# Performance work log

Hardware: AMD Instinct MI355X
Metric: run time of the kernel (lower is better)

The kernel has to match this reference:

```python
import jax, jax.numpy as jnp
import numpy as np

B, S, HID = 1, 2048, 2048
NH, NKV, HD = 32, 8, 64
SCALE = HD ** -0.5


def _rotary_tables(seq_len, dim, base=10000.0):
    inv_freq = 1.0 / (base ** (jnp.arange(0, dim, 2, dtype=jnp.float32) / dim))
    t = jnp.arange(seq_len, dtype=jnp.float32)
    freqs = jnp.outer(t, inv_freq)                      # [S, D/2]
    emb = jnp.concatenate([freqs, freqs], axis=-1)      # [S, D]
    return jnp.cos(emb)[None], jnp.sin(emb)[None]       # [1, S, D]


def setup_inputs() -> dict:
    key = jax.random.key(0)
    ks = jax.random.split(key, 5)
    cos, sin = _rotary_tables(S, HD)
    std = HID ** -0.5
    return {
        "hidden_states": jax.random.normal(ks[0], (B, S, HID), jnp.float32),
        "cos": cos,
        "sin": sin,
        "Wq": jax.random.normal(ks[1], (HID, NH * HD), jnp.float32) * std,
        "Wk": jax.random.normal(ks[2], (HID, NKV * HD), jnp.float32) * std,
        "Wv": jax.random.normal(ks[3], (HID, NKV * HD), jnp.float32) * std,
        "Wo": jax.random.normal(ks[4], (NH * HD, HID), jnp.float32) * std,
    }


def _rotate_half(x):
    x1, x2 = jnp.split(x, 2, axis=-1)
    return jnp.concatenate([-x2, x1], axis=-1)


def reference(hidden_states, cos, sin, Wq, Wk, Wv, Wo):
    b, s, _ = hidden_states.shape
    # projections -> [B, H, S, D]
    q = (hidden_states @ Wq).reshape(b, s, NH, HD).transpose(0, 2, 1, 3)
    k = (hidden_states @ Wk).reshape(b, s, NKV, HD).transpose(0, 2, 1, 3)
    v = (hidden_states @ Wv).reshape(b, s, NKV, HD).transpose(0, 2, 1, 3)
    # rotary embedding (broadcast over heads)
    c = cos[:, None, :, :]
    sn = sin[:, None, :, :]
    q = q * c + _rotate_half(q) * sn
    k = k * c + _rotate_half(k) * sn
    # GQA: repeat kv heads
    groups = NH // NKV
    k = jnp.repeat(k, groups, axis=1)
    v = jnp.repeat(v, groups, axis=1)
    scores = jnp.einsum("bhqd,bhkd->bhqk", q, k) * SCALE
    causal = jnp.tril(jnp.ones((s, s), dtype=bool))
    scores = jnp.where(causal, scores, jnp.finfo(scores.dtype).min)
    weights = jax.nn.softmax(scores, axis=-1)
    attn = jnp.einsum("bhqk,bhkd->bhqd", weights, v)
    attn = attn.transpose(0, 2, 1, 3).reshape(b, s, NH * HD)
    out = attn @ Wo
    return out, weights
```

## Files before the change

kernel.cpp:

```cpp
#include <hip/hip_runtime.h>

typedef short short8 __attribute__((ext_vector_type(8)));
typedef float f32x4 __attribute__((ext_vector_type(4)));

#define S_LEN 2048
#define HID 2048
#define NH 32
#define NKV 8
#define HD 64
#define DQKV 3072
#define SCALE 0.125f
#define SM_OFF 8.0f

static __device__ __forceinline__ unsigned short f2bf(float f) {
    unsigned int u = __float_as_uint(f);
    u += 0x7FFF + ((u >> 16) & 1);
    return (unsigned short)(u >> 16);
}
static __device__ __forceinline__ float bf2f(unsigned short u) {
    return __uint_as_float((unsigned int)u << 16);
}

#define GLDS16(g, l)                                                                     \
    __builtin_amdgcn_global_load_lds((const __attribute__((address_space(1))) unsigned int*)(g), \
                                     (__attribute__((address_space(3))) unsigned int*)(l), 16, 0, 0)

__global__ void prep(const float* __restrict__ Wq, const float* __restrict__ Wk,
                     const float* __restrict__ Wv, const float* __restrict__ Wo,
                     const float* __restrict__ hidden,
                     unsigned short* __restrict__ Wt, unsigned short* __restrict__ Wot,
                     unsigned short* __restrict__ Hb) {
    const int z = blockIdx.z;
    const int t = threadIdx.x;
    if (z == 4) {
        int idx = (blockIdx.y * 64 + blockIdx.x) * 256 + t;
        float4 v = ((const float4*)hidden)[idx];
        ushort4 o = {f2bf(v.x), f2bf(v.y), f2bf(v.z), f2bf(v.w)};
        ((ushort4*)Hb)[idx] = o;
        return;
    }
    const float* src; unsigned short* dst; int sld;
    if (z == 0)      { src = Wq; dst = Wt; sld = HID; }
    else if (z == 1) { if (blockIdx.x >= 16) return; src = Wk; dst = Wt + (size_t)2048 * HID; sld = 512; }
    else if (z == 2) { if (blockIdx.x >= 16) return; src = Wv; dst = Wt + (size_t)2560 * HID; sld = 512; }
    else             { src = Wo; dst = Wot; sld = HID; }
    __shared__ float tile[32][33];
    const int tx = t & 31, ty = t >> 5;
    const int r0 = blockIdx.y * 32, c0 = blockIdx.x * 32;
#pragma unroll
    for (int i = 0; i < 4; ++i)
        tile[ty * 4 + i][tx] = src[(size_t)(r0 + ty * 4 + i) * sld + c0 + tx];
    __syncthreads();
#pragma unroll
    for (int i = 0; i < 4; ++i)
        dst[(size_t)(c0 + ty * 4 + i) * HID + r0 + tx] = f2bf(tile[tx][ty * 4 + i]);
}

template <int MODE>
__global__ __launch_bounds__(512) void gemm_fused(const unsigned short* __restrict__ A,
                                                  const unsigned short* __restrict__ Bt,
                                                  float* __restrict__ C,
                                                  const float* __restrict__ cosb,
                                                  const float* __restrict__ sinb,
                                                  unsigned short* __restrict__ Qb,
                                                  unsigned short* __restrict__ Kb,
                                                  unsigned short* __restrict__ Vt,
                                                  int K, int lda, int ldb, int ldc) {
    __shared__ __align__(16) unsigned short As[128 * 64];
    __shared__ __align__(16) unsigned short Bs[128 * 64];
    const int t = threadIdx.x, lane = t & 63, wv = t >> 6;
    const int m0 = blockIdx.y * 128, n0 = blockIdx.x * 128;
    const int wm = wv >> 1, wn = wv & 1;
    const int lr = lane & 15, lg = lane >> 4;
    const int srow = lane >> 3;
    const int scol = ((lane & 7) ^ srow) * 8;
    f32x4 acc[2][4] = {};
    for (int k0 = 0; k0 < K; k0 += 64) {
        __syncthreads();
#pragma unroll
        for (int p = 0; p < 2; ++p) {
            int rbase = wv * 16 + p * 8;
            GLDS16(&A[(size_t)(m0 + rbase + srow) * lda + k0 + scol], &As[rbase * 64]);
            GLDS16(&Bt[(size_t)(n0 + rbase + srow) * ldb + k0 + scol], &Bs[rbase * 64]);
        }
        __syncthreads();
#pragma unroll
        for (int kk = 0; kk < 2; ++kk) {
            short8 a[2], b[4];
#pragma unroll
            for (int i = 0; i < 2; ++i) {
                int row = wm * 32 + i * 16 + lr;
                a[i] = *(const short8*)&As[row * 64 + (((kk * 4 + lg) ^ (row & 7)) * 8)];
            }
#pragma unroll
            for (int j = 0; j < 4; ++j) {
                int row = wn * 64 + j * 16 + lr;
                b[j] = *(const short8*)&Bs[row * 64 + (((kk * 4 + lg) ^ (row & 7)) * 8)];
            }
#pragma unroll
            for (int i = 0; i < 2; ++i)
#pragma unroll
                for (int j = 0; j < 4; ++j)
                    acc[i][j] = __builtin_amdgcn_mfma_f32_16x16x32_bf16(a[i], b[j], acc[i][j], 0, 0, 0);
        }
    }

    if (MODE == 1) {
#pragma unroll
        for (int i = 0; i < 2; ++i)
#pragma unroll
            for (int j = 0; j < 4; ++j)
#pragma unroll
                for (int r = 0; r < 4; ++r)
                    C[(size_t)(m0 + wm * 32 + i * 16 + lg * 4 + r) * ldc +
                      n0 + wn * 64 + j * 16 + lr] = acc[i][j][r];
        return;
    }

    const int head = (n0 + wn * 64) >> 6;
    if (head < NH + NKV) {
        unsigned short* dst = (head < NH) ? Qb : Kb;
        const int dld = (head < NH) ? HID : 512;
        const int hc = (head < NH) ? head * HD : (head - NH) * HD;
#pragma unroll
        for (int i = 0; i < 2; ++i) {
            const int s0 = m0 + wm * 32 + i * 16 + lg * 4;
#pragma unroll
            for (int j = 0; j < 2; ++j) {
                const int c = j * 16 + lr;
#pragma unroll
                for (int r = 0; r < 4; ++r) {
                    const int s = s0 + r;
                    float x1 = acc[i][j][r], x2 = acc[i][j + 2][r];
                    float c1 = cosb[s * HD + c],      s1 = sinb[s * HD + c];
                    float c2 = cosb[s * HD + c + 32], s2 = sinb[s * HD + c + 32];
                    dst[(size_t)s * dld + hc + c]      = f2bf(x1 * c1 - x2 * s1);
                    dst[(size_t)s * dld + hc + c + 32] = f2bf(x2 * c2 + x1 * s2);
                }
            }
        }
    } else {
        const int vh = head - NH - NKV;
#pragma unroll
        for (int i = 0; i < 2; ++i) {
            const int s0 = m0 + wm * 32 + i * 16 + lg * 4;
#pragma unroll
            for (int j = 0; j < 4; ++j) {
                const int d = vh * HD + j * 16 + lr;
                ushort4 o = {f2bf(acc[i][j][0]), f2bf(acc[i][j][1]),
                             f2bf(acc[i][j][2]), f2bf(acc[i][j][3])};
                *(ushort4*)&Vt[(size_t)d * S_LEN + s0] = o;
            }
        }
    }
}

#define KSZ (128 * 72)
#define VSZ (64 * 136)
__global__ __launch_bounds__(512) void attn_fused(const unsigned short* __restrict__ Qb,
                                                  const unsigned short* __restrict__ Kb,
                                                  const unsigned short* __restrict__ Vt,
                                                  float* __restrict__ w,
                                                  unsigned short* __restrict__ Ab) {
    __shared__ __align__(16) unsigned short Ks[2 * KSZ];
    __shared__ __align__(16) unsigned short Vs[2 * VSZ];
    __shared__ __align__(16) unsigned short Ps[8][32 * 40];
    const int p = blockIdx.x, h = blockIdx.y, kvh = h >> 2;
    const int t = threadIdx.x, lane = t & 63, wv = t >> 6;
    const int grp = wv & 1, wr = wv >> 1;
    const int qt = grp ? (15 - p) : p;
    const int q0 = qt * 128;
    const int lr = lane & 15, lg = lane >> 4;
    const int ktmax = 15 - p;
    unsigned short* Pw = &Ps[wv][0];

    const float C1 = SCALE;
    const float NEG = -1.0e30f;

    short8 qf[2][2];
#pragma unroll
    for (int i = 0; i < 2; ++i)
#pragma unroll
        for (int kk = 0; kk < 2; ++kk)
            qf[i][kk] = *(const short8*)&Qb[(size_t)(q0 + wr * 32 + i * 16 + lr) * HID +
                                            h * HD + kk * 32 + lg * 8];

    const int krow = t >> 2, kc = (t & 3) * 16;
    const int vrow = t >> 3, vc = (t & 7) * 16;

    short8 kA, kB, vA, vB;
#define LOADK(kt) { const unsigned short* kp = &Kb[(size_t)((kt) * 128 + krow) * 512 + kvh * HD]; \
                    kA = *(const short8*)&kp[kc]; kB = *(const short8*)&kp[kc + 8]; }
#define WRITEK(b) { *(short8*)&Ks[(b) * KSZ + krow * 72 + kc] = kA;                 \
                    *(short8*)&Ks[(b) * KSZ + krow * 72 + kc + 8] = kB; }
#define LOADV(kt) { const unsigned short* vp = &Vt[(size_t)(kvh * HD + vrow) * S_LEN + (kt) * 128]; \
                    vA = *(const short8*)&vp[vc]; vB = *(const short8*)&vp[vc + 8]; }
#define WRITEV(b) { *(short8*)&Vs[(b) * VSZ + vrow * 136 + vc] = vA;                \
                    *(short8*)&Vs[(b) * VSZ + vrow * 136 + vc + 8] = vB; }

    float l_r[2] = {0.f, 0.f};

    LOADK(0); WRITEK(0);
    __syncthreads();
    LOADK(1);
    for (int kt = 0; kt <= ktmax; ++kt) {
        const int b = kt & 1;
        if (kt <= qt) {
            f32x4 acc[8][2] = {};
#pragma unroll
            for (int kk = 0; kk < 2; ++kk) {
                short8 af[8];
#pragma unroll
                for (int j = 0; j < 8; ++j)
                    af[j] = *(const short8*)&Ks[b * KSZ + (j * 16 + lr) * 72 + kk * 32 + lg * 8];
#pragma unroll
                for (int j = 0; j < 8; ++j)
#pragma unroll
                    for (int i = 0; i < 2; ++i)
                        acc[j][i] = __builtin_amdgcn_mfma_f32_16x16x32_bf16(af[j], qf[i][kk], acc[j][i], 0, 0, 0);
            }
            const bool diag = (kt == qt);
#pragma unroll
            for (int i = 0; i < 2; ++i) {
                const int qg = q0 + wr * 32 + i * 16 + lr;
                float sum = 0.f;
#pragma unroll
                for (int j = 0; j < 8; ++j)
#pragma unroll
                    for (int r = 0; r < 4; ++r) {
                        int kg = kt * 128 + j * 16 + lg * 4 + r;
                        float s2 = fmaf(acc[j][i][r], C1, -SM_OFF);
                        s2 = (!diag || kg <= qg) ? s2 : NEG;
                        sum += __expf(s2);
                    }
                sum += __shfl_xor(sum, 16);
                sum += __shfl_xor(sum, 32);
                l_r[i] += sum;
            }
        }
        if (kt < ktmax) WRITEK(b ^ 1);
        __syncthreads();
        if (kt + 2 <= ktmax) LOADK(kt + 2);
    }

    const float invl[2] = {1.f / l_r[0], 1.f / l_r[1]};

    f32x4 o[2][4] = {};
    LOADK(0); LOADV(0); WRITEK(0); WRITEV(0);
    __syncthreads();
    LOADK(1); LOADV(1);
    for (int kt = 0; kt <= ktmax; ++kt) {
        const int b = kt & 1;
        if (kt <= qt) {
            f32x4 acc[8][2] = {};
#pragma unroll
            for (int kk = 0; kk < 2; ++kk) {
                short8 af[8];
#pragma unroll
                for (int j = 0; j < 8; ++j)
                    af[j] = *(const short8*)&Ks[b * KSZ + (j * 16 + lr) * 72 + kk * 32 + lg * 8];
#pragma unroll
                for (int j = 0; j < 8; ++j)
#pragma unroll
                    for (int i = 0; i < 2; ++i)
                        acc[j][i] = __builtin_amdgcn_mfma_f32_16x16x32_bf16(af[j], qf[i][kk], acc[j][i], 0, 0, 0);
            }
            const bool diag = (kt == qt);
#pragma unroll
            for (int ks = 0; ks < 4; ++ks) {
#pragma unroll
                for (int i = 0; i < 2; ++i) {
                    const int qg = q0 + wr * 32 + i * 16 + lr;
#pragma unroll
                    for (int jj = 0; jj < 2; ++jj) {
                        const int j = ks * 2 + jj;
                        ushort4 pk;
#pragma unroll
                        for (int r = 0; r < 4; ++r) {
                            int kg = kt * 128 + j * 16 + lg * 4 + r;
                            float s2 = fmaf(acc[j][i][r], C1, -SM_OFF);
                            s2 = (!diag || kg <= qg) ? s2 : NEG;
                            ((unsigned short*)&pk)[r] = f2bf(__expf(s2) * invl[i]);
                        }
                        *(ushort4*)&Pw[(i * 16 + lr) * 40 + jj * 16 + lg * 4] = pk;
                    }
                }
                short8 pa[2], vb[4];
#pragma unroll
                for (int i = 0; i < 2; ++i)
                    pa[i] = *(const short8*)&Pw[(i * 16 + lr) * 40 + lg * 8];
#pragma unroll
                for (int j2 = 0; j2 < 4; ++j2)
                    vb[j2] = *(const short8*)&Vs[b * VSZ + (j2 * 16 + lr) * 136 + ks * 32 + lg * 8];
#pragma unroll
                for (int i = 0; i < 2; ++i)
#pragma unroll
                    for (int j2 = 0; j2 < 4; ++j2)
                        o[i][j2] = __builtin_amdgcn_mfma_f32_16x16x32_bf16(pa[i], vb[j2], o[i][j2], 0, 0, 0);
#pragma unroll
                for (int rp = 0; rp < 2; ++rp) {
                    int rq = (lane >> 2) + rp * 16;
                    int cb = (lane & 3) * 8;
                    short8 pv8 = *(const short8*)&Pw[rq * 40 + cb];
                    f32x4 f0 = {bf2f((unsigned short)pv8[0]), bf2f((unsigned short)pv8[1]),
                                bf2f((unsigned short)pv8[2]), bf2f((unsigned short)pv8[3])};
                    f32x4 f1 = {bf2f((unsigned short)pv8[4]), bf2f((unsigned short)pv8[5]),
                                bf2f((unsigned short)pv8[6]), bf2f((unsigned short)pv8[7])};
                    size_t base = ((size_t)h * S_LEN + q0 + wr * 32 + rq) * S_LEN + kt * 128 + ks * 32 + cb;
                    *(f32x4*)&w[base] = f0;
                    *(f32x4*)&w[base + 4] = f1;
                }
            }
        } else {
            f32x4 z4 = {0.f, 0.f, 0.f, 0.f};
#pragma unroll
            for (int rr = 0; rr < 16; ++rr) {
                int row = wr * 32 + rr * 2 + (lane >> 5);
                *(f32x4*)&w[((size_t)h * S_LEN + q0 + row) * S_LEN + kt * 128 + (lane & 31) * 4] = z4;
            }
        }
        if (kt < ktmax) { WRITEK(b ^ 1); WRITEV(b ^ 1); }
        __syncthreads();
        if (kt + 2 <= ktmax) { LOADK(kt + 2); LOADV(kt + 2); }
    }
    for (int kt = ktmax + 1; kt < 16; ++kt) {
        f32x4 z4 = {0.f, 0.f, 0.f, 0.f};
#pragma unroll
        for (int rr = 0; rr < 16; ++rr) {
            int row = wr * 32 + rr * 2 + (lane >> 5);
            *(f32x4*)&w[((size_t)h * S_LEN + q0 + row) * S_LEN + kt * 128 + (lane & 31) * 4] = z4;
        }
    }
#pragma unroll
    for (int i = 0; i < 2; ++i)
#pragma unroll
        for (int j2 = 0; j2 < 4; ++j2)
#pragma unroll
            for (int r = 0; r < 4; ++r)
                Ab[(size_t)(q0 + wr * 32 + i * 16 + lg * 4 + r) * HID +
                   h * HD + j2 * 16 + lr] = f2bf(o[i][j2][r]);
}

extern "C" void kernel_launch(void* const* d_in, const int* in_sizes, int n_in,
                              void* d_out, int out_size, void* d_ws, size_t ws_size,
                              hipStream_t stream) {
    const float* hidden = (const float*)d_in[0];
    const float* cosb   = (const float*)d_in[1];
    const float* sinb   = (const float*)d_in[2];
    const float* Wq     = (const float*)d_in[3];
    const float* Wk     = (const float*)d_in[4];
    const float* Wv     = (const float*)d_in[5];
    const float* Wo     = (const float*)d_in[6];

    float* out_mat = (float*)d_out;
    float* weights = (float*)d_out + (size_t)S_LEN * HID;

    char* wsb = (char*)d_ws;
    unsigned short* Hb  = (unsigned short*)wsb;
    unsigned short* Wt  = (unsigned short*)(wsb + (size_t)8  * 1024 * 1024);
    unsigned short* Wot = (unsigned short*)(wsb + (size_t)20 * 1024 * 1024);
    unsigned short* Qb  = (unsigned short*)(wsb + (size_t)28 * 1024 * 1024);
    unsigned short* Kb  = (unsigned short*)(wsb + (size_t)36 * 1024 * 1024);
    unsigned short* Vt  = (unsigned short*)(wsb + (size_t)38 * 1024 * 1024);
    unsigned short* Ab  = (unsigned short*)(wsb + (size_t)40 * 1024 * 1024);

    prep<<<dim3(64, 64, 5), 256, 0, stream>>>(Wq, Wk, Wv, Wo, hidden, Wt, Wot, Hb);

    gemm_fused<0><<<dim3(DQKV / 128, S_LEN / 128), 512, 0, stream>>>(
        Hb, Wt, nullptr, cosb, sinb, Qb, Kb, Vt, HID, HID, HID, 0);

    attn_fused<<<dim3(8, NH), 512, 0, stream>>>(Qb, Kb, Vt, weights, Ab);

    gemm_fused<1><<<dim3(HID / 128, S_LEN / 128), 512, 0, stream>>>(
        Ab, Wot, out_mat, nullptr, nullptr, nullptr, nullptr, nullptr, HID, HID, HID, HID);
}
```

Baseline: 260.8 us.

## Single-buffer K/V LDS and interleave QK per j-tile to raise occupancy

Replaces double-buffered K/V shared memory with single buffers, loaded into registers one tile ahead and written under two barriers per iteration. The QK^T score computation is restructured to process one 16-key slice at a time instead of holding all 8 accumulator tiles and fragments, cutting register pressure. Launch bounds now request 4 blocks per SM. The aim is higher occupancy to hide latency, at the cost of an extra barrier per tile and less overlap between LDS writes and compute.

```diff
diff --git a/kernel.cpp b/kernel.cpp
--- a/kernel.cpp
+++ b/kernel.cpp
@@ -155,15 +155,13 @@
     }
 }
 
-#define KSZ (128 * 72)
-#define VSZ (64 * 136)
-__global__ __launch_bounds__(512) void attn_fused(const unsigned short* __restrict__ Qb,
-                                                  const unsigned short* __restrict__ Kb,
-                                                  const unsigned short* __restrict__ Vt,
-                                                  float* __restrict__ w,
-                                                  unsigned short* __restrict__ Ab) {
-    __shared__ __align__(16) unsigned short Ks[2 * KSZ];
-    __shared__ __align__(16) unsigned short Vs[2 * VSZ];
+__global__ __launch_bounds__(512, 4) void attn_fused(const unsigned short* __restrict__ Qb,
+                                                     const unsigned short* __restrict__ Kb,
+                                                     const unsigned short* __restrict__ Vt,
+                                                     float* __restrict__ w,
+                                                     unsigned short* __restrict__ Ab) {
+    __shared__ __align__(16) unsigned short Ks[128 * 72];
+    __shared__ __align__(16) unsigned short Vs[64 * 136];
     __shared__ __align__(16) unsigned short Ps[8][32 * 40];
     const int p = blockIdx.x, h = blockIdx.y, kvh = h >> 2;
     const int t = threadIdx.x, lane = t & 63, wv = t >> 6;
@@ -173,8 +171,6 @@
     const int lr = lane & 15, lg = lane >> 4;
     const int ktmax = 15 - p;
     unsigned short* Pw = &Ps[wv][0];
-
-    const float C1 = SCALE;
     const float NEG = -1.0e30f;
 
     short8 qf[2][2];
@@ -191,94 +187,85 @@
     short8 kA, kB, vA, vB;
 #define LOADK(kt) { const unsigned short* kp = &Kb[(size_t)((kt) * 128 + krow) * 512 + kvh * HD]; \
                     kA = *(const short8*)&kp[kc]; kB = *(const short8*)&kp[kc + 8]; }
-#define WRITEK(b) { *(short8*)&Ks[(b) * KSZ + krow * 72 + kc] = kA;                 \
-                    *(short8*)&Ks[(b) * KSZ + krow * 72 + kc + 8] = kB; }
+#define WRITEK()  { *(short8*)&Ks[krow * 72 + kc] = kA;                 \
+                    *(short8*)&Ks[krow * 72 + kc + 8] = kB; }
 #define LOADV(kt) { const unsigned short* vp = &Vt[(size_t)(kvh * HD + vrow) * S_LEN + (kt) * 128]; \
                     vA = *(const short8*)&vp[vc]; vB = *(const short8*)&vp[vc + 8]; }
-#define WRITEV(b) { *(short8*)&Vs[(b) * VSZ + vrow * 136 + vc] = vA;                \
-                    *(short8*)&Vs[(b) * VSZ + vrow * 136 + vc + 8] = vB; }
+#define WRITEV()  { *(short8*)&Vs[vrow * 136 + vc] = vA;                \
+                    *(short8*)&Vs[vrow * 136 + vc + 8] = vB; }
 
     float l_r[2] = {0.f, 0.f};
 
-    LOADK(0); WRITEK(0);
-    __syncthreads();
-    LOADK(1);
+    LOADK(0);
     for (int kt = 0; kt <= ktmax; ++kt) {
-        const int b = kt & 1;
-        if (kt <= qt) {
-            f32x4 acc[8][2] = {};
+        __syncthreads();
+        WRITEK();
+        __syncthreads();
+        if (kt < ktmax) LOADK(kt + 1);
+        if (kt > qt) continue;
+        const bool diag = (kt == qt);
+        float sum0 = 0.f, sum1 = 0.f;
+#pragma unroll
+        for (int j = 0; j < 8; ++j) {
+            f32x4 acc[2] = {};
 #pragma unroll
             for (int kk = 0; kk < 2; ++kk) {
-                short8 af[8];
-#pragma unroll
-                for (int j = 0; j < 8; ++j)
-                    af[j] = *(const short8*)&Ks[b * KSZ + (j * 16 + lr) * 72 + kk * 32 + lg * 8];
-#pragma unroll
-                for (int j = 0; j < 8; ++j)
-#pragma unroll
-                    for (int i = 0; i < 2; ++i)
-                        acc[j][i] = __builtin_amdgcn_mfma_f32_16x16x32_bf16(af[j], qf[i][kk], acc[j][i], 0, 0, 0);
-            }
-            const bool diag = (kt == qt);
+                short8 af = *(const short8*)&Ks[(j * 16 + lr) * 72 + kk * 32 + lg * 8];
+#pragma unroll
+                for (int i = 0; i < 2; ++i)
+                    acc[i] = __builtin_amdgcn_mfma_f32_16x16x32_bf16(af, qf[i][kk], acc[i], 0, 0, 0);
+            }
 #pragma unroll
             for (int i = 0; i < 2; ++i) {
                 const int qg = q0 + wr * 32 + i * 16 + lr;
-                float sum = 0.f;
-#pragma unroll
-                for (int j = 0; j < 8; ++j)
-#pragma unroll
-                    for (int r = 0; r < 4; ++r) {
-                        int kg = kt * 128 + j * 16 + lg * 4 + r;
-                        float s2 = fmaf(acc[j][i][r], C1, -SM_OFF);
-                        s2 = (!diag || kg <= qg) ? s2 : NEG;
-                        sum += __expf(s2);
+                float ps = 0.f;
+#pragma unroll
+                for (int r = 0; r < 4; ++r) {
+                    int kg = kt * 128 + j * 16 + lg * 4 + r;
+                    float s2 = fmaf(acc[i][r], SCALE, -SM_OFF);
+                    s2 = (!diag || kg <= qg) ? s2 : NEG;
+                    ps += __expf(s2);
+                }
+                if (i == 0) sum0 += ps; else sum1 += ps;
+            }
+        }
+        sum0 += __shfl_xor(sum0, 16); sum0 += __shfl_xor(sum0, 32);
+        sum1 += __shfl_xor(sum1, 16); sum1 += __shfl_xor(sum1, 32);
+        l_r[0] += sum0; l_r[1] += sum1;
+    }
+
+    const float invl[2] = {1.f / l_r[0], 1.f / l_r[1]};
+
+    f32x4 o[2][4] = {};
+    LOADK(0); LOADV(0);
+    for (int kt = 0; kt <= ktmax; ++kt) {
+        __syncthreads();
+        WRITEK(); WRITEV();
+        __syncthreads();
+        if (kt < ktmax) { LOADK(kt + 1); LOADV(kt + 1); }
+        if (kt <= qt) {
+            const bool diag = (kt == qt);
+#pragma unroll
+            for (int ks = 0; ks < 4; ++ks) {
+#pragma unroll
+                for (int jj = 0; jj < 2; ++jj) {
+                    const int j = ks * 2 + jj;
+                    f32x4 acc[2] = {};
+#pragma unroll
+                    for (int kk = 0; kk < 2; ++kk) {
+                        short8 af = *(const short8*)&Ks[(j * 16 + lr) * 72 + kk * 32 + lg * 8];
+#pragma unroll
+                        for (int i = 0; i < 2; ++i)
+                            acc[i] = __builtin_amdgcn_mfma_f32_16x16x32_bf16(af, qf[i][kk], acc[i], 0, 0, 0);
                     }
-                sum += __shfl_xor(sum, 16);
-                sum += __shfl_xor(sum, 32);
-                l_r[i] += sum;
-            }
-        }
-        if (kt < ktmax) WRITEK(b ^ 1);
-        __syncthreads();
-        if (kt + 2 <= ktmax) LOADK(kt + 2);
-    }
-
-    const float invl[2] = {1.f / l_r[0], 1.f / l_r[1]};
-
-    f32x4 o[2][4] = {};
-    LOADK(0); LOADV(0); WRITEK(0); WRITEV(0);
-    __syncthreads();
-    LOADK(1); LOADV(1);
-    for (int kt = 0; kt <= ktmax; ++kt) {
-        const int b = kt & 1;
-        if (kt <= qt) {
-            f32x4 acc[8][2] = {};
-#pragma unroll
-            for (int kk = 0; kk < 2; ++kk) {
-                short8 af[8];
-#pragma unroll
-                for (int j = 0; j < 8; ++j)
-                    af[j] = *(const short8*)&Ks[b * KSZ + (j * 16 + lr) * 72 + kk * 32 + lg * 8];
-#pragma unroll
-                for (int j = 0; j < 8; ++j)
-#pragma unroll
-                    for (int i = 0; i < 2; ++i)
-                        acc[j][i] = __builtin_amdgcn_mfma_f32_16x16x32_bf16(af[j], qf[i][kk], acc[j][i], 0, 0, 0);
-            }
-            const bool diag = (kt == qt);
-#pragma unroll
-            for (int ks = 0; ks < 4; ++ks) {
-#pragma unroll
-                for (int i = 0; i < 2; ++i) {
-                    const int qg = q0 + wr * 32 + i * 16 + lr;
-#pragma unroll
-                    for (int jj = 0; jj < 2; ++jj) {
-                        const int j = ks * 2 + jj;
+#pragma unroll
+                    for (int i = 0; i < 2; ++i) {
+                        const int qg = q0 + wr * 32 + i * 16 + lr;
                         ushort4 pk;
 #pragma unroll
                         for (int r = 0; r < 4; ++r) {
                             int kg = kt * 128 + j * 16 + lg * 4 + r;
-                            float s2 = fmaf(acc[j][i][r], C1, -SM_OFF);
+                            float s2 = fmaf(acc[i][r], SCALE, -SM_OFF);
                             s2 = (!diag || kg <= qg) ? s2 : NEG;
                             ((unsigned short*)&pk)[r] = f2bf(__expf(s2) * invl[i]);
                         }
@@ -291,7 +278,7 @@
                     pa[i] = *(const short8*)&Pw[(i * 16 + lr) * 40 + lg * 8];
 #pragma unroll
                 for (int j2 = 0; j2 < 4; ++j2)
-                    vb[j2] = *(const short8*)&Vs[b * VSZ + (j2 * 16 + lr) * 136 + ks * 32 + lg * 8];
+                    vb[j2] = *(const short8*)&Vs[(j2 * 16 + lr) * 136 + ks * 32 + lg * 8];
 #pragma unroll
                 for (int i = 0; i < 2; ++i)
 #pragma unroll
@@ -319,9 +306,6 @@
                 *(f32x4*)&w[((size_t)h * S_LEN + q0 + row) * S_LEN + kt * 128 + (lane & 31) * 4] = z4;
             }
         }
-        if (kt < ktmax) { WRITEK(b ^ 1); WRITEV(b ^ 1); }
-        __syncthreads();
-        if (kt + 2 <= ktmax) { LOADK(kt + 2); LOADV(kt + 2); }
     }
     for (int kt = ktmax + 1; kt < 16; ++kt) {
         f32x4 z4 = {0.f, 0.f, 0.f, 0.f};
```

Result: slower. 293.3 us (+12.5%).
